# Optimization experiments

Hardware: AMD Instinct MI355X
Metric: run time of the kernel (lower is better)

The kernel has to match this reference:

```python
import jax, jax.numpy as jnp
import numpy as np
from jax import lax
from jax.scipy.special import logsumexp

B, T, N = 256, 512, 128


def setup_inputs() -> dict:
    key = jax.random.key(0)
    k1, k2, k3 = jax.random.split(key, 3)
    emissions = jax.random.normal(k1, (B, T, N), dtype=jnp.float32)
    tag_ids = jax.random.randint(k2, (B, T), 0, N, dtype=jnp.int64)
    mask = jnp.ones((B, T), dtype=jnp.int32)
    # learned transition matrix (glorot-uniform-ish init)
    limit = float(np.sqrt(6.0 / (N + N)))
    trans = jax.random.uniform(k3, (N, N), minval=-limit, maxval=limit, dtype=jnp.float32)
    return {"emissions": emissions, "tag_ids": tag_ids, "mask": mask, "trans": trans}


def _sequence_score(emissions, tag_ids, maskf, trans):
    # unary: emission score of the gold tag at each valid step
    unary = jnp.take_along_axis(emissions, tag_ids[:, :, None], axis=2)[..., 0]  # [B,T]
    unary = jnp.sum(unary * maskf, axis=1)
    # binary: transition score between consecutive gold tags
    binary = trans[tag_ids[:, :-1], tag_ids[:, 1:]] * maskf[:, 1:]  # [B,T-1]
    return unary + jnp.sum(binary, axis=1)


def _log_norm(emissions, maskf, trans):
    # forward algorithm over time via lax.scan; alpha: [B,N]
    alpha0 = emissions[:, 0]
    em = jnp.swapaxes(emissions, 0, 1)[1:]   # [T-1,B,N]
    mk = jnp.swapaxes(maskf, 0, 1)[1:]       # [T-1,B]

    def step(alpha, xs):
        emit_t, m_t = xs
        new = logsumexp(alpha[:, :, None] + trans[None], axis=1) + emit_t
        alpha = jnp.where(m_t[:, None] > 0, new, alpha)
        return alpha, None

    alpha, _ = lax.scan(step, alpha0, (em, mk))
    return logsumexp(alpha, axis=1)  # [B]


def _viterbi_decode(emissions, maskf, trans):
    alpha0 = emissions[:, 0]
    em = jnp.swapaxes(emissions, 0, 1)[1:]
    mk = jnp.swapaxes(maskf, 0, 1)[1:]
    idx = jnp.arange(N, dtype=jnp.int32)[None]

    def fwd(alpha, xs):
        emit_t, m_t = xs
        scores = alpha[:, :, None] + trans[None]        # [B,N,N]
        bp = jnp.argmax(scores, axis=1).astype(jnp.int32)  # [B,N]
        new = jnp.max(scores, axis=1) + emit_t
        valid = m_t[:, None] > 0
        alpha = jnp.where(valid, new, alpha)
        bp = jnp.where(valid, bp, idx)  # carry same tag through padding
        return alpha, bp

    alpha, bps = lax.scan(fwd, alpha0, (em, mk))  # bps: [T-1,B,N]
    last_tag = jnp.argmax(alpha, axis=1).astype(jnp.int32)  # [B]

    def bwd(tag, bp_t):
        new_tag = jnp.take_along_axis(bp_t, tag[:, None], axis=1)[:, 0]
        return new_tag, new_tag

    _, tags_rev = lax.scan(bwd, last_tag, bps[::-1])  # [T-1,B]
    tags = jnp.concatenate([tags_rev[::-1], last_tag[None]], axis=0)  # [T,B]
    return jnp.swapaxes(tags, 0, 1)  # [B,T]


def reference(emissions, tag_ids, mask, trans):
    maskf = mask.astype(emissions.dtype)
    log_likelihood = _sequence_score(emissions, tag_ids, maskf, trans) - _log_norm(emissions, maskf, trans)
    predict = _viterbi_decode(emissions, maskf, trans)
    return (log_likelihood, trans, predict)
```

## Files before the change

kernel.cpp:

```cpp
#include <hip/hip_runtime.h>
#include <cmath>

#define BB 256
#define TT 512
#define NN 128
#define LN2F 0.6931471805599453f

typedef __bf16 bf16x8 __attribute__((ext_vector_type(8)));
typedef float floatx4 __attribute__((ext_vector_type(4)));

__device__ __forceinline__ float wave_max64(float v) {
    #pragma unroll
    for (int off = 32; off; off >>= 1) v = fmaxf(v, __shfl_xor(v, off));
    return v;
}
__device__ __forceinline__ float wave_sum64(float v) {
    #pragma unroll
    for (int off = 32; off; off >>= 1) v += __shfl_xor(v, off);
    return v;
}
__device__ __forceinline__ int wave_argmax128(float v0, float v1, int l) {
    float m = fmaxf(v0, v1);
    float wm = wave_max64(m);
    unsigned long long ball = __ballot(m == wm);
    int lane = __ffsll(ball) - 1;
    int idx = (v0 == wm) ? (2 * l) : (2 * l + 1);
    return __shfl(idx, lane);
}

__device__ __forceinline__ __bf16 to_bf16(float f) {
    unsigned u = __float_as_uint(f);
    unsigned r = (u + 0x7FFFu + ((u >> 16) & 1u)) >> 16;
    union { unsigned short s; __bf16 b; } cv;
    cv.s = (unsigned short)r;
    return cv.b;
}

__device__ __forceinline__ float dpp_xor1_f(float v) {
    return __int_as_float(__builtin_amdgcn_mov_dpp(__float_as_int(v), 0xB1, 0xF, 0xF, true));
}
__device__ __forceinline__ int dpp_xor1_i(int v) {
    return __builtin_amdgcn_mov_dpp(v, 0xB1, 0xF, 0xF, true);
}
__device__ __forceinline__ float dpp_xor2_f(float v) {
    return __int_as_float(__builtin_amdgcn_mov_dpp(__float_as_int(v), 0x4E, 0xF, 0xF, true));
}
__device__ __forceinline__ int dpp_xor2_i(int v) {
    return __builtin_amdgcn_mov_dpp(v, 0x4E, 0xF, 0xF, true);
}

__device__ __forceinline__ int padidx(int i) { return 36 * (i >> 5) + (i & 31); }

__global__ __launch_bounds__(512, 4) void fwd_kernel(
        const float* __restrict__ em, const int* __restrict__ gtags,
        const int* __restrict__ mask, const float* __restrict__ trans,
        float* __restrict__ out_ll, float* __restrict__ out_trans,
        float* __restrict__ outp) {
    const int bi = blockIdx.x;
    const bool isV = bi < BB;
    const int b = isV ? bi : bi - BB;
    const int tid = threadIdx.x;
    const int w = tid >> 6;
    const int l = tid & 63;

    __shared__ __align__(16) float stA[144], stB[144];
    __shared__ __align__(16) __bf16 sbf[2][NN];
    __shared__ unsigned char bp_lds[TT * NN];
    __shared__ unsigned char tags_lds[TT];
    __shared__ unsigned char map_lds[8 * NN];
    __shared__ int entry_sh[8];
    __shared__ int msk[TT];
    __shared__ float piv[2];
    __shared__ float sfin[NN];
    __shared__ float wsum[8];
    __shared__ float llnorm_sh;
    __shared__ int misc[2];

    msk[tid] = mask[b * TT + tid];

    const float* emb = em + (size_t)b * TT * NN;

    if (isV) {
        __builtin_amdgcn_s_setprio(1);
        const int jv = (l >> 2) + 16 * w;
        const int qv = l & 3;
        const int i0 = 32 * qv;
        float4 c0, c1, c2, c3, c4, c5, c6, c7;
        {
            const float* tc = trans + (size_t)i0 * NN + jv;
            #define LDC(cc, u) cc.x = tc[(4*u+0)*NN]; cc.y = tc[(4*u+1)*NN]; \
                               cc.z = tc[(4*u+2)*NN]; cc.w = tc[(4*u+3)*NN];
            LDC(c0, 0) LDC(c1, 1) LDC(c2, 2) LDC(c3, 3)
            LDC(c4, 4) LDC(c5, 5) LDC(c6, 6) LDC(c7, 7)
            #undef LDC
        }
        float st = 0.f;
        {
            float a0 = emb[jv];
            st = a0;
            if ((l & 3) == 0) stA[padidx(jv)] = a0;
        }
        float e_next = emb[NN + jv];
        __syncthreads();

        unsigned long long mb = __ballot(msk[l] != 0);

        const float4* apA = (const float4*)(stA + 36 * qv);
        const float4* apB = (const float4*)(stB + 36 * qv);

        auto VSTEP = [&](int t, const float4* ap, float* dst) {
            if ((t & 63) == 0) mb = __ballot(msk[t + l] != 0);
            const int m = (int)((mb >> (t & 63)) & 1ULL);
            const float e_cur = e_next;
            if (t + 1 < TT) e_next = emb[(size_t)(t + 1) * NN + jv];
            float4 v0 = ap[0], v1 = ap[1], v2 = ap[2], v3 = ap[3],
                   v4 = ap[4], v5 = ap[5], v6 = ap[6], v7 = ap[7];
            float m0 = -INFINITY, m1 = -INFINITY, m2 = -INFINITY, m3 = -INFINITY;
            int u0 = 0, u1 = 0, u2 = 0, u3 = 0;
            #define CH(vv, cc, u) { \
                float a = vv.x + cc.x; u0 = (a > m0) ? u : u0; m0 = fmaxf(m0, a); \
                float bq = vv.y + cc.y; u1 = (bq > m1) ? u : u1; m1 = fmaxf(m1, bq); \
                float c = vv.z + cc.z; u2 = (c > m2) ? u : u2; m2 = fmaxf(m2, c); \
                float d = vv.w + cc.w; u3 = (d > m3) ? u : u3; m3 = fmaxf(m3, d); }
            CH(v0, c0, 0) CH(v1, c1, 1) CH(v2, c2, 2) CH(v3, c3, 3)
            CH(v4, c4, 4) CH(v5, c5, 5) CH(v6, c6, 6) CH(v7, c7, 7)
            #undef CH
            float bv = m0; int bx = i0 + 4 * u0;
            { int id = i0 + 4*u1 + 1; if (m1 > bv || (m1 == bv && id < bx)) { bv = m1; bx = id; } }
            { int id = i0 + 4*u2 + 2; if (m2 > bv || (m2 == bv && id < bx)) { bv = m2; bx = id; } }
            { int id = i0 + 4*u3 + 3; if (m3 > bv || (m3 == bv && id < bx)) { bv = m3; bx = id; } }
            {
                float ov = dpp_xor1_f(bv); int oi = dpp_xor1_i(bx);
                if (ov > bv || (ov == bv && oi < bx)) { bv = ov; bx = oi; }
                ov = dpp_xor2_f(bv); oi = dpp_xor2_i(bx);
                if (ov > bv || (ov == bv && oi < bx)) { bv = ov; bx = oi; }
            }
            if ((l & 3) == 0) {
                float an; int bp;
                if (m) { an = bv + e_cur; bp = bx; }
                else   { an = st;         bp = jv; }
                st = an;
                dst[padidx(jv)] = an;
                bp_lds[t * NN + jv] = (unsigned char)bp;
            }
            __syncthreads();
        };

        for (int t = 1; t < TT - 1; t += 2) {
            VSTEP(t, apA, stB);
            VSTEP(t + 1, apB, stA);
        }
        VSTEP(TT - 1, apA, stB);

        if (w == 0) {
            float a0 = stB[padidx(2 * l)], a1 = stB[padidx(2 * l + 1)];
            int tg = wave_argmax128(a0, a1, l);
            if (l == 0) { misc[0] = tg; tags_lds[TT - 1] = (unsigned char)tg; }
        }
        if (tid < 64) out_trans[b * 64 + tid] = trans[b * 64 + tid];
        __syncthreads();
        const int lo = 64 * w + 1;
        const int hi = (w == 7) ? (TT - 1) : (64 * w + 64);
        {
            int tA = 2 * l, tB = 2 * l + 1;
            for (int t = hi; t >= lo; --t) {
                tA = bp_lds[t * NN + tA];
                tB = bp_lds[t * NN + tB];
            }
            map_lds[w * NN + 2 * l]     = (unsigned char)tA;
            map_lds[w * NN + 2 * l + 1] = (unsigned char)tB;
        }
        __syncthreads();
        if (tid == 0) {
            int e = misc[0];
            entry_sh[7] = e;
            for (int c = 7; c >= 1; --c) { e = map_lds[c * NN + e]; entry_sh[c - 1] = e; }
        }
        __syncthreads();
        if (l == 0) {
            int tg = entry_sh[w];
            for (int t = hi; t >= lo; --t) {
                tg = bp_lds[t * NN + tg];
                tags_lds[t - 1] = (unsigned char)tg;
            }
        }
        __syncthreads();
        outp[(size_t)b * TT + tid] = (float)tags_lds[tid];
        __builtin_amdgcn_s_setprio(0);
    } else {
        const int j = (l & 15) + 16 * w;
        const int q = l >> 4;
        bf16x8 Bf[4];
        #pragma unroll
        for (int kc = 0; kc < 4; ++kc) {
            #pragma unroll
            for (int jj = 0; jj < 8; ++jj) {
                int row = kc * 32 + q * 8 + jj;
                Bf[kc][jj] = to_bf16(__expf(trans[(size_t)row * NN + j]));
            }
        }
        float ss = __expf(emb[j]);
        int kacc = 0;
        if (l < 16) sbf[0][j] = to_bf16(ss);
        if (tid == 0) piv[0] = ss;
        float e_next = emb[NN + j];
        __syncthreads();

        for (int t = 1; t < TT; ++t) {
            const float e_cur = e_next;
            if (t + 1 < TT) e_next = emb[(size_t)(t + 1) * NN + j];
            const int m = msk[t];
            const int p = (t - 1) & 1, qb = t & 1;
            if (m) {
                const __bf16* sp = sbf[p];
                floatx4 acc = {0.f, 0.f, 0.f, 0.f};
                #pragma unroll
                for (int kc = 0; kc < 4; ++kc) {
                    bf16x8 a = *(const bf16x8*)(sp + kc * 32 + q * 8);
                    acc = __builtin_amdgcn_mfma_f32_16x16x32_bf16(a, Bf[kc], acc, 0, 0, 0);
                }
                float dot = acc[0];
                const float pv = piv[p];
                const int k = (int)(__float_as_uint(pv) >> 23) - 127;
                const float scale = __uint_as_float((unsigned)(127 - k) << 23);
                ss = dot * scale * __expf(e_cur);
                if (tid == 0) kacc += k;
            }
            if (l < 16) sbf[qb][j] = to_bf16(ss);
            if (tid == 0) piv[qb] = ss;
            __syncthreads();
        }

        if (l < 16) sfin[j] = ss;
        if (tid == 0) misc[1] = kacc;
        __syncthreads();
        if (w == 0) {
            float v = sfin[2 * l] + sfin[2 * l + 1];
            v = wave_sum64(v);
            if (l == 0) llnorm_sh = __logf(v) + (float)misc[1] * LN2F;
        }
        float acc = 0.f;
        {
            int tg = gtags[b * TT + tid];
            float mf = (float)msk[tid];
            acc = emb[(size_t)tid * NN + tg] * mf;
            if (tid >= 1) {
                int tp = gtags[b * TT + tid - 1];
                acc += trans[tp * NN + tg] * mf;
            }
        }
        acc = wave_sum64(acc);
        if (l == 0) wsum[w] = acc;
        __syncthreads();
        if (tid == 0) {
            float s = 0.f;
            #pragma unroll
            for (int i = 0; i < 8; ++i) s += wsum[i];
            out_ll[b] = s - llnorm_sh;
        }
    }
}

extern "C" void kernel_launch(void* const* d_in, const int* in_sizes, int n_in,
                              void* d_out, int out_size, void* d_ws, size_t ws_size,
                              hipStream_t stream) {
    const float* em = (const float*)d_in[0];
    const int* gtags = (const int*)d_in[1];
    const int* mask = (const int*)d_in[2];
    const float* trans = (const float*)d_in[3];

    float* out = (float*)d_out;
    float* out_ll = out;
    float* out_trans = out + BB;
    float* out_pred = out + BB + NN * NN;

    hipLaunchKernelGGL(fwd_kernel, dim3(2 * BB), dim3(512), 0, stream,
                       em, gtags, mask, trans, out_ll, out_trans, out_pred);
}
```

Before: 503.1 us.

## Halve block size to 256 threads, doubling per-thread work in both paths

```diff
diff --git a/kernel.cpp b/kernel.cpp
--- a/kernel.cpp
+++ b/kernel.cpp
@@ -42,16 +42,10 @@
 __device__ __forceinline__ int dpp_xor1_i(int v) {
     return __builtin_amdgcn_mov_dpp(v, 0xB1, 0xF, 0xF, true);
 }
-__device__ __forceinline__ float dpp_xor2_f(float v) {
-    return __int_as_float(__builtin_amdgcn_mov_dpp(__float_as_int(v), 0x4E, 0xF, 0xF, true));
-}
-__device__ __forceinline__ int dpp_xor2_i(int v) {
-    return __builtin_amdgcn_mov_dpp(v, 0x4E, 0xF, 0xF, true);
-}
-
-__device__ __forceinline__ int padidx(int i) { return 36 * (i >> 5) + (i & 31); }
-
-__global__ __launch_bounds__(512, 4) void fwd_kernel(
+
+__device__ __forceinline__ int padidx64(int i) { return 68 * (i >> 6) + (i & 63); }
+
+__global__ __launch_bounds__(256, 2) void fwd_kernel(
         const float* __restrict__ em, const int* __restrict__ gtags,
         const int* __restrict__ mask, const float* __restrict__ trans,
         float* __restrict__ out_ll, float* __restrict__ out_trans,
@@ -63,68 +57,71 @@
     const int w = tid >> 6;
     const int l = tid & 63;
 
-    __shared__ __align__(16) float stA[144], stB[144];
+    __shared__ __align__(16) float stA[136], stB[136];
     __shared__ __align__(16) __bf16 sbf[2][NN];
     __shared__ unsigned char bp_lds[TT * NN];
     __shared__ unsigned char tags_lds[TT];
-    __shared__ unsigned char map_lds[8 * NN];
-    __shared__ int entry_sh[8];
+    __shared__ unsigned char map_lds[4 * NN];
+    __shared__ int entry_sh[4];
     __shared__ int msk[TT];
     __shared__ float piv[2];
     __shared__ float sfin[NN];
-    __shared__ float wsum[8];
+    __shared__ float wsum[4];
     __shared__ float llnorm_sh;
     __shared__ int misc[2];
 
     msk[tid] = mask[b * TT + tid];
+    msk[tid + 256] = mask[b * TT + tid + 256];
 
     const float* emb = em + (size_t)b * TT * NN;
 
     if (isV) {
         __builtin_amdgcn_s_setprio(1);
-        const int jv = (l >> 2) + 16 * w;
-        const int qv = l & 3;
-        const int i0 = 32 * qv;
-        float4 c0, c1, c2, c3, c4, c5, c6, c7;
+        const int jv = tid >> 1;
+        const int qv = tid & 1;
+        const int i0 = 64 * qv;
+        float4 C[16];
         {
             const float* tc = trans + (size_t)i0 * NN + jv;
-            #define LDC(cc, u) cc.x = tc[(4*u+0)*NN]; cc.y = tc[(4*u+1)*NN]; \
-                               cc.z = tc[(4*u+2)*NN]; cc.w = tc[(4*u+3)*NN];
-            LDC(c0, 0) LDC(c1, 1) LDC(c2, 2) LDC(c3, 3)
-            LDC(c4, 4) LDC(c5, 5) LDC(c6, 6) LDC(c7, 7)
-            #undef LDC
-        }
-        float st = 0.f;
+            #pragma unroll
+            for (int u = 0; u < 16; ++u) {
+                C[u].x = tc[(size_t)(4*u+0) * NN];
+                C[u].y = tc[(size_t)(4*u+1) * NN];
+                C[u].z = tc[(size_t)(4*u+2) * NN];
+                C[u].w = tc[(size_t)(4*u+3) * NN];
+            }
+        }
+        float st;
         {
             float a0 = emb[jv];
             st = a0;
-            if ((l & 3) == 0) stA[padidx(jv)] = a0;
+            if (qv == 0) stA[padidx64(jv)] = a0;
         }
         float e_next = emb[NN + jv];
         __syncthreads();
 
         unsigned long long mb = __ballot(msk[l] != 0);
 
-        const float4* apA = (const float4*)(stA + 36 * qv);
-        const float4* apB = (const float4*)(stB + 36 * qv);
+        const float4* apA = (const float4*)(stA + 68 * qv);
+        const float4* apB = (const float4*)(stB + 68 * qv);
 
         auto VSTEP = [&](int t, const float4* ap, float* dst) {
             if ((t & 63) == 0) mb = __ballot(msk[t + l] != 0);
             const int m = (int)((mb >> (t & 63)) & 1ULL);
             const float e_cur = e_next;
             if (t + 1 < TT) e_next = emb[(size_t)(t + 1) * NN + jv];
-            float4 v0 = ap[0], v1 = ap[1], v2 = ap[2], v3 = ap[3],
-                   v4 = ap[4], v5 = ap[5], v6 = ap[6], v7 = ap[7];
+            float4 vv[16];
+            #pragma unroll
+            for (int u = 0; u < 16; ++u) vv[u] = ap[u];
             float m0 = -INFINITY, m1 = -INFINITY, m2 = -INFINITY, m3 = -INFINITY;
             int u0 = 0, u1 = 0, u2 = 0, u3 = 0;
-            #define CH(vv, cc, u) { \
-                float a = vv.x + cc.x; u0 = (a > m0) ? u : u0; m0 = fmaxf(m0, a); \
-                float bq = vv.y + cc.y; u1 = (bq > m1) ? u : u1; m1 = fmaxf(m1, bq); \
-                float c = vv.z + cc.z; u2 = (c > m2) ? u : u2; m2 = fmaxf(m2, c); \
-                float d = vv.w + cc.w; u3 = (d > m3) ? u : u3; m3 = fmaxf(m3, d); }
-            CH(v0, c0, 0) CH(v1, c1, 1) CH(v2, c2, 2) CH(v3, c3, 3)
-            CH(v4, c4, 4) CH(v5, c5, 5) CH(v6, c6, 6) CH(v7, c7, 7)
-            #undef CH
+            #pragma unroll
+            for (int u = 0; u < 16; ++u) {
+                float a = vv[u].x + C[u].x; u0 = (a > m0) ? u : u0; m0 = fmaxf(m0, a);
+                float bq = vv[u].y + C[u].y; u1 = (bq > m1) ? u : u1; m1 = fmaxf(m1, bq);
+                float c = vv[u].z + C[u].z; u2 = (c > m2) ? u : u2; m2 = fmaxf(m2, c);
+                float d = vv[u].w + C[u].w; u3 = (d > m3) ? u : u3; m3 = fmaxf(m3, d);
+            }
             float bv = m0; int bx = i0 + 4 * u0;
             { int id = i0 + 4*u1 + 1; if (m1 > bv || (m1 == bv && id < bx)) { bv = m1; bx = id; } }
             { int id = i0 + 4*u2 + 2; if (m2 > bv || (m2 == bv && id < bx)) { bv = m2; bx = id; } }
@@ -132,15 +129,13 @@
             {
                 float ov = dpp_xor1_f(bv); int oi = dpp_xor1_i(bx);
                 if (ov > bv || (ov == bv && oi < bx)) { bv = ov; bx = oi; }
-                ov = dpp_xor2_f(bv); oi = dpp_xor2_i(bx);
-                if (ov > bv || (ov == bv && oi < bx)) { bv = ov; bx = oi; }
-            }
-            if ((l & 3) == 0) {
+            }
+            if (qv == 0) {
                 float an; int bp;
                 if (m) { an = bv + e_cur; bp = bx; }
                 else   { an = st;         bp = jv; }
                 st = an;
-                dst[padidx(jv)] = an;
+                dst[padidx64(jv)] = an;
                 bp_lds[t * NN + jv] = (unsigned char)bp;
             }
             __syncthreads();
@@ -153,14 +148,14 @@
         VSTEP(TT - 1, apA, stB);
 
         if (w == 0) {
-            float a0 = stB[padidx(2 * l)], a1 = stB[padidx(2 * l + 1)];
+            float a0 = stB[padidx64(2 * l)], a1 = stB[padidx64(2 * l + 1)];
             int tg = wave_argmax128(a0, a1, l);
             if (l == 0) { misc[0] = tg; tags_lds[TT - 1] = (unsigned char)tg; }
         }
         if (tid < 64) out_trans[b * 64 + tid] = trans[b * 64 + tid];
         __syncthreads();
-        const int lo = 64 * w + 1;
-        const int hi = (w == 7) ? (TT - 1) : (64 * w + 64);
+        const int lo = 128 * w + 1;
+        const int hi = (w == 3) ? (TT - 1) : (128 * w + 128);
         {
             int tA = 2 * l, tB = 2 * l + 1;
             for (int t = hi; t >= lo; --t) {
@@ -173,8 +168,8 @@
         __syncthreads();
         if (tid == 0) {
             int e = misc[0];
-            entry_sh[7] = e;
-            for (int c = 7; c >= 1; --c) { e = map_lds[c * NN + e]; entry_sh[c - 1] = e; }
+            entry_sh[3] = e;
+            for (int c = 3; c >= 1; --c) { e = map_lds[c * NN + e]; entry_sh[c - 1] = e; }
         }
         __syncthreads();
         if (l == 0) {
@@ -185,53 +180,63 @@
             }
         }
         __syncthreads();
-        outp[(size_t)b * TT + tid] = (float)tags_lds[tid];
+        outp[(size_t)b * TT + tid]       = (float)tags_lds[tid];
+        outp[(size_t)b * TT + tid + 256] = (float)tags_lds[tid + 256];
         __builtin_amdgcn_s_setprio(0);
     } else {
-        const int j = (l & 15) + 16 * w;
         const int q = l >> 4;
-        bf16x8 Bf[4];
+        const int j0 = (l & 15) + 32 * w;
+        const int j1 = j0 + 16;
+        bf16x8 Bf0[4], Bf1[4];
         #pragma unroll
         for (int kc = 0; kc < 4; ++kc) {
             #pragma unroll
             for (int jj = 0; jj < 8; ++jj) {
                 int row = kc * 32 + q * 8 + jj;
-                Bf[kc][jj] = to_bf16(__expf(trans[(size_t)row * NN + j]));
-            }
-        }
-        float ss = __expf(emb[j]);
+                Bf0[kc][jj] = to_bf16(__expf(trans[(size_t)row * NN + j0]));
+                Bf1[kc][jj] = to_bf16(__expf(trans[(size_t)row * NN + j1]));
+            }
+        }
+        float ss0 = __expf(emb[j0]);
+        float ss1 = __expf(emb[j1]);
         int kacc = 0;
-        if (l < 16) sbf[0][j] = to_bf16(ss);
-        if (tid == 0) piv[0] = ss;
-        float e_next = emb[NN + j];
+        if (l < 16) { sbf[0][j0] = to_bf16(ss0); sbf[0][j1] = to_bf16(ss1); }
+        if (tid == 0) piv[0] = ss0;
+        float e0_next = emb[NN + j0];
+        float e1_next = emb[NN + j1];
         __syncthreads();
 
         for (int t = 1; t < TT; ++t) {
-            const float e_cur = e_next;
-            if (t + 1 < TT) e_next = emb[(size_t)(t + 1) * NN + j];
+            const float e0_cur = e0_next, e1_cur = e1_next;
+            if (t + 1 < TT) {
+                e0_next = emb[(size_t)(t + 1) * NN + j0];
+                e1_next = emb[(size_t)(t + 1) * NN + j1];
+            }
             const int m = msk[t];
             const int p = (t - 1) & 1, qb = t & 1;
             if (m) {
                 const __bf16* sp = sbf[p];
-                floatx4 acc = {0.f, 0.f, 0.f, 0.f};
+                floatx4 acc0 = {0.f, 0.f, 0.f, 0.f};
+                floatx4 acc1 = {0.f, 0.f, 0.f, 0.f};
                 #pragma unroll
                 for (int kc = 0; kc < 4; ++kc) {
                     bf16x8 a = *(const bf16x8*)(sp + kc * 32 + q * 8);
-                    acc = __builtin_amdgcn_mfma_f32_16x16x32_bf16(a, Bf[kc], acc, 0, 0, 0);
+                    acc0 = __builtin_amdgcn_mfma_f32_16x16x32_bf16(a, Bf0[kc], acc0, 0, 0, 0);
+                    acc1 = __builtin_amdgcn_mfma_f32_16x16x32_bf16(a, Bf1[kc], acc1, 0, 0, 0);
                 }
-                float dot = acc[0];
                 const float pv = piv[p];
                 const int k = (int)(__float_as_uint(pv) >> 23) - 127;
                 const float scale = __uint_as_float((unsigned)(127 - k) << 23);
-                ss = dot * scale * __expf(e_cur);
+                ss0 = acc0[0] * scale * __expf(e0_cur);
+                ss1 = acc1[0] * scale * __expf(e1_cur);
                 if (tid == 0) kacc += k;
             }
-            if (l < 16) sbf[qb][j] = to_bf16(ss);
-            if (tid == 0) piv[qb] = ss;
+            if (l < 16) { sbf[qb][j0] = to_bf16(ss0); sbf[qb][j1] = to_bf16(ss1); }
+            if (tid == 0) piv[qb] = ss0;
             __syncthreads();
         }
 
-        if (l < 16) sfin[j] = ss;
+        if (l < 16) { sfin[j0] = ss0; sfin[j1] = ss1; }
         if (tid == 0) misc[1] = kacc;
         __syncthreads();
         if (w == 0) {
@@ -240,12 +245,14 @@
             if (l == 0) llnorm_sh = __logf(v) + (float)misc[1] * LN2F;
         }
         float acc = 0.f;
-        {
-            int tg = gtags[b * TT + tid];
-            float mf = (float)msk[tid];
-            acc = emb[(size_t)tid * NN + tg] * mf;
-            if (tid >= 1) {
-                int tp = gtags[b * TT + tid - 1];
+        #pragma unroll
+        for (int rep = 0; rep < 2; ++rep) {
+            int t = tid + rep * 256;
+            int tg = gtags[b * TT + t];
+            float mf = (float)msk[t];
+            acc += em[((size_t)b * TT + t) * NN + tg] * mf;
+            if (t >= 1) {
+                int tp = gtags[b * TT + t - 1];
                 acc += trans[tp * NN + tg] * mf;
             }
         }
@@ -255,7 +262,7 @@
         if (tid == 0) {
             float s = 0.f;
             #pragma unroll
-            for (int i = 0; i < 8; ++i) s += wsum[i];
+            for (int i = 0; i < 4; ++i) s += wsum[i];
             out_ll[b] = s - llnorm_sh;
         }
     }
@@ -274,6 +281,6 @@
     float* out_trans = out + BB;
     float* out_pred = out + BB + NN * NN;
 
-    hipLaunchKernelGGL(fwd_kernel, dim3(2 * BB), dim3(512), 0, stream,
+    hipLaunchKernelGGL(fwd_kernel, dim3(2 * BB), dim3(256), 0, stream,
                        em, gtags, mask, trans, out_ll, out_trans, out_pred);
 }
```

Measured after the change: 580.2 us. 1.15x slower.
